# Optimization experiments

Measured on AMD Instinct MI355X. Metric: run time of the kernel, lower is better.

The kernel has to match this reference:

```python
import jax, jax.numpy as jnp
import numpy as np
import math

EMB, QK, V, HEAD = 512, 64, 64, 8
B, S = 8, 2048

def setup_inputs() -> dict:
    key = jax.random.key(0)
    ks = jax.random.split(key, 10)
    sc = 1.0 / math.sqrt(EMB)
    return {
        "x_q": jax.random.normal(ks[0], (B, S, EMB), jnp.float32),
        "x_k_v": jax.random.normal(ks[1], (B, S, EMB), jnp.float32),
        "attn_mask": jax.random.randint(ks[2], (B, S, S), 0, 2, jnp.int32),
        "w_q": jax.random.normal(ks[3], (HEAD * QK, EMB), jnp.float32) * sc,
        "b_q": jax.random.normal(ks[4], (HEAD * QK,), jnp.float32) * sc,
        "w_k": jax.random.normal(ks[5], (HEAD * QK, EMB), jnp.float32) * sc,
        "b_k": jax.random.normal(ks[6], (HEAD * QK,), jnp.float32) * sc,
        "w_v": jax.random.normal(ks[7], (HEAD * V, EMB), jnp.float32) * sc,
        "b_v": jax.random.normal(ks[8], (HEAD * V,), jnp.float32) * sc,
    }

def reference(x_q, x_k_v, attn_mask, w_q, b_q, w_k, b_k, w_v, b_v):
    Bq, Sq, _ = x_q.shape
    Skv = x_k_v.shape[1]
    # linear projections (torch Linear: x @ W.T + b)
    q = (x_q @ w_q.T + b_q).reshape(Bq, Sq, HEAD, QK)     # [B,Sq,H,Dk]
    k = (x_k_v @ w_k.T + b_k).reshape(Bq, Skv, HEAD, QK)  # [B,Skv,H,Dk]
    v = (x_k_v @ w_v.T + b_v).reshape(Bq, Skv, HEAD, V)   # [B,Skv,H,Dv]
    # scores [B,H,Sq,Skv]
    attn = jnp.einsum("bqhd,bkhd->bhqk", q, k) / math.sqrt(QK)
    mask = attn_mask[:, None, :, :].astype(bool)
    attn = jnp.where(mask, jnp.float32(-1e9), attn)
    attn = jax.nn.softmax(attn, axis=-1)
    z = jnp.einsum("bhqk,bkhd->bqhd", attn, v)            # [B,Sq,H,Dv]
    return z.reshape(Bq, Sq, HEAD * V)
```

## Files before the change

### kernel.cpp

```cpp
#include <hip/hip_runtime.h>
#include <hip/hip_bf16.h>
#include <math.h>

typedef float  f32x4  __attribute__((ext_vector_type(4)));
typedef float  f32x16 __attribute__((ext_vector_type(16)));
typedef short  s16x8  __attribute__((ext_vector_type(8)));
typedef __bf16 bf16x8 __attribute__((ext_vector_type(8)));
typedef unsigned int u32;
typedef unsigned int u32x4 __attribute__((ext_vector_type(4)));
typedef unsigned short u16;
typedef unsigned long long u64;

#define DEVI static __device__ __forceinline__

#if defined(__has_builtin) && __has_builtin(__builtin_amdgcn_exp2f)
#define EXP2(x) __builtin_amdgcn_exp2f(x)
#else
#define EXP2(x) exp2f(x)
#endif

DEVI u32 cvtpk(float lo, float hi) {
  u32 r;
  asm("v_cvt_pk_bf16_f32 %0, %1, %2" : "=v"(r) : "v"(lo), "v"(hi));
  return r;
}

DEVI f32x4 mfma_bf16(s16x8 a, s16x8 b, f32x4 c) {
  return __builtin_amdgcn_mfma_f32_16x16x32_bf16(
      __builtin_bit_cast(bf16x8, a), __builtin_bit_cast(bf16x8, b), c, 0, 0, 0);
}

DEVI f32x16 mfma32(s16x8 a, s16x8 b, f32x16 c) {
  return __builtin_amdgcn_mfma_f32_32x32x16_bf16(
      __builtin_bit_cast(bf16x8, a), __builtin_bit_cast(bf16x8, b), c, 0, 0, 0);
}

DEVI void gload_lds16(const void* g, void* l) {
  __builtin_amdgcn_global_load_lds(
      (const __attribute__((address_space(1))) void*)g,
      (__attribute__((address_space(3))) void*)l, 16, 0, 0);
}

__global__ __launch_bounds__(256)
void mask_pack(const int* __restrict__ mask, u64* __restrict__ mp,
               const float* __restrict__ wq, const float* __restrict__ wk,
               const float* __restrict__ wv, u16* __restrict__ Wbf) {
  const int t = threadIdx.x, lane = t & 63;
  if (blockIdx.x >= 8192) {
    const u32 blk = blockIdx.x - 8192;
    const u32 g0 = blk * 4096 + (u32)t * 16;
    const u32 mtx = g0 >> 18;
    const float* src = (mtx == 0) ? wq : (mtx == 1 ? wk : wv);
    const u32 idx = g0 & 262143u;
    #pragma unroll
    for (int i = 0; i < 2; ++i) {
      f32x4 v0 = *(const f32x4*)(src + idx + i * 8);
      f32x4 v1 = *(const f32x4*)(src + idx + i * 8 + 4);
      u32x4 pk;
      pk[0] = cvtpk(v0[0], v0[1]); pk[1] = cvtpk(v0[2], v0[3]);
      pk[2] = cvtpk(v1[0], v1[1]); pk[3] = cvtpk(v1[2], v1[3]);
      *(u32x4*)(Wbf + (size_t)mtx * 262144 + idx + i * 8) = pk;
    }
    return;
  }
  const u32 gw = blockIdx.x * 4 + (t >> 6);
  const u32 W0 = gw * 16;
  #define MSRC(W) ((((size_t)((W) >> 16) * 2048 + ((W) & 2047u)) * 2048) \
                   + (((W) >> 11) & 31u) * 64 + lane)
  int c0 = mask[MSRC(W0)];
  int c1 = mask[MSRC(W0 + 1)];
  #pragma unroll 4
  for (u32 k = 0; k < 16; ++k) {
    u64 bits = __ballot(c0 == 0);
    if (lane == 0) mp[W0 + k] = bits;
    c0 = c1;
    if (k + 2 < 16) c1 = mask[MSRC(W0 + k + 2)];
  }
  #undef MSRC
}

__global__ __launch_bounds__(256, 2)
void qkv_proj(const float* __restrict__ xq, const float* __restrict__ xkv,
              const u16* __restrict__ Wbf,
              const float* __restrict__ bq, const float* __restrict__ bk,
              const float* __restrict__ bv,
              u16* __restrict__ Qo, u16* __restrict__ Ko, u16* __restrict__ VTo)
{
  __shared__ __align__(16) char smem[57344];
  char* a32 = smem;
  char* bbf = smem + 32768;
  char* abf = smem + 49152;

  const int t = threadIdx.x, lane = t & 63, w = t >> 6;
  const int z = blockIdx.z;
  const float* X  = (z == 0) ? xq : xkv;
  const u16*   W  = Wbf + (size_t)z * 262144;
  const float* Bv = (z == 0) ? bq : (z == 1 ? bk : bv);

  const int m0 = blockIdx.x * 128, n0 = blockIdx.y * 128;
  const int wr = w >> 1, wc = w & 1, g = lane >> 4, q15 = lane & 15;
  const int srow = t >> 1, shalf = t & 1;

  f32x4 acc[4][4];
  #pragma unroll
  for (int i = 0; i < 4; ++i)
    #pragma unroll
    for (int j = 0; j < 4; ++j) acc[i][j] = (f32x4){0.f, 0.f, 0.f, 0.f};

  const float* aSrc[4];
  int aDst[4];
  #pragma unroll
  for (int i = 0; i < 4; ++i) {
    int c = w * 256 + i * 64 + lane;
    int r = c >> 3, s = c & 7, j = s ^ (r & 7);
    aSrc[i] = X + (size_t)(m0 + r) * 512 + j * 4;
    aDst[i] = (w * 256 + i * 64) * 16;
  }
  const u16* bSrc[2];
  int bDst[2];
  #pragma unroll
  for (int i = 0; i < 2; ++i) {
    int c = i * 256 + w * 64 + lane;
    int r = c >> 2, s = c & 3, j = s ^ (r & 3);
    bSrc[i] = W + (size_t)(n0 + r) * 512 + j * 8;
    bDst[i] = (i * 256 + w * 64) * 16;
  }

  #pragma unroll
  for (int i = 0; i < 4; ++i) gload_lds16(aSrc[i], a32 + aDst[i]);
  #pragma unroll
  for (int i = 0; i < 2; ++i) gload_lds16(bSrc[i], bbf + bDst[i]);
  asm volatile("" ::: "memory");

  const int wbyte = srow * 64;
  const int sw = (srow & 3) << 4;

  #pragma unroll 1
  for (int kt = 0; kt < 16; ++kt) {
    const int cur = kt & 1;
    if (kt + 1 < 16) {
      #pragma unroll
      for (int i = 0; i < 4; ++i) {
        aSrc[i] += 32;
        gload_lds16(aSrc[i], a32 + (cur ^ 1) * 16384 + aDst[i]);
      }
      #pragma unroll
      for (int i = 0; i < 2; ++i) {
        bSrc[i] += 32;
        gload_lds16(bSrc[i], bbf + (cur ^ 1) * 8192 + bDst[i]);
      }
      asm volatile("" ::: "memory");
      asm volatile("s_waitcnt vmcnt(6)" ::: "memory");
    } else {
      asm volatile("s_waitcnt vmcnt(0)" ::: "memory");
    }
    asm volatile("s_waitcnt lgkmcnt(0)" ::: "memory");
    __builtin_amdgcn_sched_barrier(0);
    asm volatile("s_barrier" ::: "memory");

    {
      const char* base = a32 + cur * 16384 + srow * 128;
      f32x4 av[4];
      #pragma unroll
      for (int jj = 0; jj < 4; ++jj) {
        int slot = (shalf * 4 + jj) ^ (srow & 7);
        av[jj] = *(const f32x4*)(base + slot * 16);
      }
      const float* pf = (const float*)av;
      #pragma unroll
      for (int half = 0; half < 2; ++half) {
        u32x4 wa;
        #pragma unroll
        for (int e2 = 0; e2 < 4; ++e2)
          wa[e2] = cvtpk(pf[half * 8 + 2 * e2], pf[half * 8 + 2 * e2 + 1]);
        *(u32x4*)(abf + wbyte + ((shalf * 32 + half * 16) ^ sw)) = wa;
      }
    }
    asm volatile("s_waitcnt lgkmcnt(0)" ::: "memory");
    __builtin_amdgcn_sched_barrier(0);
    asm volatile("s_barrier" ::: "memory");

    s16x8 afr[4], bfr[4];
    #pragma unroll
    for (int mi = 0; mi < 4; ++mi) {
      int row = wr * 64 + mi * 16 + q15;
      afr[mi] = *(const s16x8*)(abf + row * 64 + ((g * 16) ^ ((row & 3) << 4)));
    }
    #pragma unroll
    for (int ni = 0; ni < 4; ++ni) {
      int row = wc * 64 + ni * 16 + q15;
      bfr[ni] = *(const s16x8*)(bbf + cur * 8192 + row * 64 + ((g * 16) ^ ((row & 3) << 4)));
    }
    #pragma unroll
    for (int mi = 0; mi < 4; ++mi)
      #pragma unroll
      for (int ni = 0; ni < 4; ++ni)
        acc[mi][ni] = mfma_bf16(afr[mi], bfr[ni], acc[mi][ni]);
  }

  float bias[4];
  #pragma unroll
  for (int ni = 0; ni < 4; ++ni) bias[ni] = Bv[n0 + wc * 64 + ni * 16 + q15];

  if (z < 2) {
    u16* Out = z ? Ko : Qo;
    const float scale = z ? 1.0f : 0.18033688011112042f;
    #pragma unroll
    for (int mi = 0; mi < 4; ++mi)
      #pragma unroll
      for (int ni = 0; ni < 4; ++ni)
        #pragma unroll
        for (int r = 0; r < 4; r += 2) {
          int m = m0 + wr * 64 + mi * 16 + g * 4 + r;
          int n = n0 + wc * 64 + ni * 16 + q15;
          u32 pk = cvtpk((acc[mi][ni][r] + bias[ni]) * scale,
                         (acc[mi][ni][r + 1] + bias[ni]) * scale);
          Out[(size_t)m * 512 + n]       = (u16)pk;
          Out[(size_t)(m + 1) * 512 + n] = (u16)(pk >> 16);
        }
  } else {
    __syncthreads();
    #pragma unroll
    for (int mi = 0; mi < 4; ++mi)
      #pragma unroll
      for (int ni = 0; ni < 4; ++ni)
        #pragma unroll
        for (int r = 0; r < 4; r += 2) {
          int ml = wr * 64 + mi * 16 + g * 4 + r;
          int nl = wc * 64 + ni * 16 + q15;
          *(u32*)(smem + nl * 272 + ml * 2) =
              cvtpk(acc[mi][ni][r] + bias[ni], acc[mi][ni][r + 1] + bias[ni]);
        }
    __syncthreads();
    const int b  = m0 >> 11;
    const int s0 = m0 & 2047;
    #pragma unroll
    for (int nn = 0; nn < 2; ++nn) {
      int n  = nn * 64 + (t >> 2);
      int q4 = t & 3;
      u16* dst = VTo + (size_t)(b * 512 + n0 + n) * 2048 + s0 + q4 * 32;
      #pragma unroll
      for (int jj = 0; jj < 4; ++jj)
        *(s16x8*)(dst + jj * 8) = *(const s16x8*)(smem + n * 272 + q4 * 64 + jj * 16);
    }
  }
}

__global__ __launch_bounds__(256, 2)
void attn_fwd(const u16* __restrict__ Q, const u16* __restrict__ K,
              const u16* __restrict__ VT, const u64* __restrict__ MP,
              float* __restrict__ out)
{
  __shared__ __align__(16) char lds_k[2][16384];
  __shared__ __align__(16) char lds_v[2][2][8192];

  const int bid = blockIdx.x;
  const int hh = bid & 7, b = (bid >> 3) & 7, qt = bid >> 6;
  const int t = threadIdx.x, lane = t & 63, w = t >> 6;
  const int l31 = lane & 31, hi = lane >> 5;
  const int qbase = qt * 128 + w * 32;
  const int swz = (l31 & 7) << 4;

  s16x8 qf[4];
  #pragma unroll
  for (int j = 0; j < 4; ++j)
    qf[j] = *(const s16x8*)(Q + (size_t)(b * 2048 + qbase + l31) * 512
                              + hh * 64 + j * 16 + hi * 8);
  asm volatile("" ::: "memory");

  f32x16 o0 = {0.f,0.f,0.f,0.f,0.f,0.f,0.f,0.f,0.f,0.f,0.f,0.f,0.f,0.f,0.f,0.f};
  f32x16 o1 = o0, o2 = o0;
  const f32x16 ZZ = o0;
  const s16x8 onesf = {0x3F80,0x3F80,0x3F80,0x3F80,0x3F80,0x3F80,0x3F80,0x3F80};

  const int srow8 = lane >> 3, slot = lane & 7;

  const u16* kP[4];
  int kD[4];
  #pragma unroll
  for (int i = 0; i < 4; ++i) {
    int rl = w * 32 + i * 8 + srow8;
    kP[i] = K + (size_t)(b * 2048 + rl) * 512 + hh * 64 + (slot ^ (rl & 7)) * 8;
    kD[i] = (w * 32 + i * 8) * 128;
  }
  const u16* vP[2];
  int vD[2];
  #pragma unroll
  for (int i = 0; i < 2; ++i) {
    int d = w * 16 + i * 8 + srow8;
    vP[i] = VT + (size_t)(b * 512 + hh * 64 + d) * 2048 + (slot ^ (d & 7)) * 8;
    vD[i] = (w * 16 + i * 8) * 128;
  }
  const u64* mpP = MP + (size_t)b * 32 * 2048 + qbase + l31;

  #pragma unroll
  for (int i = 0; i < 4; ++i) gload_lds16(kP[i], &lds_k[0][kD[i]]);
  #pragma unroll
  for (int hf = 0; hf < 2; ++hf)
    #pragma unroll
    for (int i = 0; i < 2; ++i)
      gload_lds16(vP[i] + hf * 64, &lds_v[0][hf][vD[i]]);
  asm volatile("" ::: "memory");
  u64 pm0 = mpP[0], pm1 = mpP[2048];

#define HALF(KB, VB, KW) do {                                                  \
    f32x16 p0 = ZZ, p1 = ZZ;                                                   \
    _Pragma("unroll")                                                          \
    for (int j = 0; j < 4; ++j) {                                              \
      s16x8 a0 = *(const s16x8*)((KB) + l31 * 128        + ((j * 32 + hi * 16) ^ swz)); \
      s16x8 a1 = *(const s16x8*)((KB) + (l31 + 32) * 128 + ((j * 32 + hi * 16) ^ swz)); \
      p0 = mfma32(a0, qf[j], p0);                                              \
      p1 = mfma32(a1, qf[j], p1);                                              \
    }                                                                          \
    u64 kws = (KW) >> (hi * 4);                                                \
    u32 mm0 = (u32)kws, mm1 = (u32)(kws >> 32);                                \
    u32 wds[16];                                                               \
    _Pragma("unroll")                                                          \
    for (int t2 = 0; t2 < 2; ++t2) {                                           \
      const u32 mmw = t2 ? mm1 : mm0;                                          \
      _Pragma("unroll")                                                        \
      for (int q2 = 0; q2 < 8; ++q2) {                                         \
        const int bp = 8 * (q2 >> 1) + 2 * (q2 & 1);                           \
        float s0v = t2 ? p1[2 * q2] : p0[2 * q2];                              \
        float s1v = t2 ? p1[2 * q2 + 1] : p0[2 * q2 + 1];                      \
        float e0 = EXP2(s0v), e1 = EXP2(s1v);                                  \
        u32 k0 = (u32)((int)(mmw << (31 - bp)) >> 31);                         \
        u32 k1 = (u32)((int)(mmw << (30 - bp)) >> 31);                         \
        e0 = __builtin_bit_cast(float, __builtin_bit_cast(u32, e0) & k0);      \
        e1 = __builtin_bit_cast(float, __builtin_bit_cast(u32, e1) & k1);      \
        wds[t2 * 8 + q2] = cvtpk(e0, e1);                                      \
      }                                                                        \
    }                                                                          \
    _Pragma("unroll")                                                          \
    for (int j = 0; j < 4; ++j) {                                              \
      const int ia = 2 * j, ib = 2 * j + 1;                                    \
      u32 wa0 = wds[(ia >> 2) * 8 + 2 * (ia & 3)];                             \
      u32 wa1 = wds[(ia >> 2) * 8 + 2 * (ia & 3) + 1];                         \
      u32 wb0 = wds[(ib >> 2) * 8 + 2 * (ib & 3)];                             \
      u32 wb1 = wds[(ib >> 2) * 8 + 2 * (ib & 3) + 1];                         \
      asm("v_permlane32_swap_b32 %0, %1" : "+v"(wa0), "+v"(wb0));              \
      asm("v_permlane32_swap_b32 %0, %1" : "+v"(wa1), "+v"(wb1));              \
      u32x4 aw = {wa0, wa1, wb0, wb1};                                         \
      s16x8 af = __builtin_bit_cast(s16x8, aw);                                \
      s16x8 v0 = *(const s16x8*)((VB) + l31 * 128        + ((j * 32 + hi * 16) ^ swz)); \
      s16x8 v1 = *(const s16x8*)((VB) + (l31 + 32) * 128 + ((j * 32 + hi * 16) ^ swz)); \
      o0 = mfma32(af, v0, o0);                                                 \
      o1 = mfma32(af, v1, o1);                                                 \
      o2 = mfma32(af, onesf, o2);                                              \
    }                                                                          \
  } while (0)

  #pragma unroll 1
  for (int kt = 0; kt < 16; ++kt) {
    const int cur = kt & 1;
    const u64 kwA = pm0, kwB = pm1;
    if (kt + 1 < 16) {
      #pragma unroll
      for (int i = 0; i < 4; ++i) kP[i] += 65536;
      #pragma unroll
      for (int i = 0; i < 2; ++i) vP[i] += 128;
      mpP += 4096;
      #pragma unroll
      for (int i = 0; i < 4; ++i) gload_lds16(kP[i], &lds_k[cur ^ 1][kD[i]]);
      #pragma unroll
      for (int hf = 0; hf < 2; ++hf)
        #pragma unroll
        for (int i = 0; i < 2; ++i)
          gload_lds16(vP[i] + hf * 64, &lds_v[cur ^ 1][hf][vD[i]]);
      asm volatile("" ::: "memory");
      pm0 = mpP[0]; pm1 = mpP[2048];
      asm volatile("s_waitcnt vmcnt(10)" ::: "memory");
    } else {
      asm volatile("s_waitcnt vmcnt(0)" ::: "memory");
    }
    asm volatile("s_barrier" ::: "memory");

    HALF(&lds_k[cur][0],    &lds_v[cur][0][0], kwA);
    HALF(&lds_k[cur][8192], &lds_v[cur][1][0], kwB);

    asm volatile("s_waitcnt lgkmcnt(0)" ::: "memory");
    __builtin_amdgcn_sched_barrier(0);
    asm volatile("s_barrier" ::: "memory");
  }
#undef HALF

  #pragma unroll
  for (int reg = 0; reg < 16; ++reg) {
    const int ql = (reg & 3) + 8 * (reg >> 2) + 4 * hi;
    const float linv = 1.0f / o2[reg];
    float* po = out + (size_t)(b * 2048 + qbase + ql) * 512 + hh * 64 + l31;
    po[0]  = o0[reg] * linv;
    po[32] = o1[reg] * linv;
  }
}

extern "C" void kernel_launch(void* const* d_in, const int* in_sizes, int n_in,
                              void* d_out, int out_size, void* d_ws, size_t ws_size,
                              hipStream_t stream) {
  const float* xq  = (const float*)d_in[0];
  const float* xkv = (const float*)d_in[1];
  const int*   msk = (const int*)d_in[2];
  const float* wq  = (const float*)d_in[3];
  const float* bq  = (const float*)d_in[4];
  const float* wk  = (const float*)d_in[5];
  const float* bk  = (const float*)d_in[6];
  const float* wv  = (const float*)d_in[7];
  const float* bv  = (const float*)d_in[8];

  u16* Qw  = (u16*)d_ws;
  u16* Kw  = Qw + (size_t)16384 * 512;
  u16* VT  = Kw + (size_t)16384 * 512;
  u64* MP  = (u64*)(VT + (size_t)4096 * 2048);
  u16* Wbf = (u16*)(MP + (size_t)8 * 32 * 2048);

  mask_pack<<<dim3(8384), 256, 0, stream>>>(msk, MP, wq, wk, wv, Wbf);
  qkv_proj<<<dim3(128, 4, 3), 256, 0, stream>>>(xq, xkv, Wbf, bq, bk, bv,
                                                Qw, Kw, VT);
  attn_fwd<<<dim3(1024), 256, 0, stream>>>(Qw, Kw, VT, MP, (float*)d_out);
}
```

Baseline: 197.7 us.

## Pre-expand mask bits into per-lane 16-bit AND words for attention

The mask-pack kernel now writes, for each 64-bit ballot, 32 per-lane u32 words that are already expanded into 0xFFFF/0 halves in the lane order the attention kernel uses. The attention kernel then ANDs the packed bf16 exponent pairs directly with these words. This drops the per-element shift/sign-extend mask extraction from the softmax inner loop, and the vmcnt waits are retuned so the mask loads are waited on only just before use. The cost is a mask buffer 32 times larger, read as 128 bytes per lane per K tile, so both kernels move more memory.

```diff
diff --git a/kernel.cpp b/kernel.cpp
--- a/kernel.cpp
+++ b/kernel.cpp
@@ -42,7 +42,7 @@
 }
 
 __global__ __launch_bounds__(256)
-void mask_pack(const int* __restrict__ mask, u64* __restrict__ mp,
+void mask_pack(const int* __restrict__ mask, u32* __restrict__ MX,
                const float* __restrict__ wq, const float* __restrict__ wk,
                const float* __restrict__ wv, u16* __restrict__ Wbf) {
   const int t = threadIdx.x, lane = t & 63;
@@ -65,6 +65,8 @@
   }
   const u32 gw = blockIdx.x * 4 + (t >> 6);
   const u32 W0 = gw * 16;
+  const int hi2 = (lane >> 4) & 1, w16 = lane & 15;
+  const int bp = 32 * (w16 >> 3) + 8 * ((w16 & 7) >> 1) + 2 * (w16 & 1) + 4 * hi2;
   #define MSRC(W) ((((size_t)((W) >> 16) * 2048 + ((W) & 2047u)) * 2048) \
                    + (((W) >> 11) & 31u) * 64 + lane)
   int c0 = mask[MSRC(W0)];
@@ -72,7 +74,12 @@
   #pragma unroll 4
   for (u32 k = 0; k < 16; ++k) {
     u64 bits = __ballot(c0 == 0);
-    if (lane == 0) mp[W0 + k] = bits;
+    if (lane < 32) {
+      u32 m0 = (u32)(bits >> bp) & 1u;
+      u32 m1 = (u32)(bits >> (bp + 1)) & 1u;
+      u32 wd = (m0 ? 0xFFFFu : 0u) | (m1 ? 0xFFFF0000u : 0u);
+      MX[(size_t)(W0 + k) * 32 + lane] = wd;
+    }
     c0 = c1;
     if (k + 2 < 16) c1 = mask[MSRC(W0 + k + 2)];
   }
@@ -248,7 +255,7 @@
 
 __global__ __launch_bounds__(256, 2)
 void attn_fwd(const u16* __restrict__ Q, const u16* __restrict__ K,
-              const u16* __restrict__ VT, const u64* __restrict__ MP,
+              const u16* __restrict__ VT, const u32* __restrict__ MX,
               float* __restrict__ out)
 {
   __shared__ __align__(16) char lds_k[2][16384];
@@ -291,7 +298,7 @@
     vP[i] = VT + (size_t)(b * 512 + hh * 64 + d) * 2048 + (slot ^ (d & 7)) * 8;
     vD[i] = (w * 16 + i * 8) * 128;
   }
-  const u64* mpP = MP + (size_t)b * 32 * 2048 + qbase + l31;
+  const u32* mxP = MX + ((size_t)(b * 32) * 2048 + qbase + l31) * 32 + hi * 16;
 
   #pragma unroll
   for (int i = 0; i < 4; ++i) gload_lds16(kP[i], &lds_k[0][kD[i]]);
@@ -301,9 +308,8 @@
     for (int i = 0; i < 2; ++i)
       gload_lds16(vP[i] + hf * 64, &lds_v[0][hf][vD[i]]);
   asm volatile("" ::: "memory");
-  u64 pm0 = mpP[0], pm1 = mpP[2048];
-
-#define HALF(KB, VB, KW) do {                                                  \
+
+#define HALF(KB, VB, MW, WAITASM) do {                                         \
     f32x16 p0 = ZZ, p1 = ZZ;                                                   \
     _Pragma("unroll")                                                          \
     for (int j = 0; j < 4; ++j) {                                              \
@@ -312,25 +318,19 @@
       p0 = mfma32(a0, qf[j], p0);                                              \
       p1 = mfma32(a1, qf[j], p1);                                              \
     }                                                                          \
-    u64 kws = (KW) >> (hi * 4);                                                \
-    u32 mm0 = (u32)kws, mm1 = (u32)(kws >> 32);                                \
     u32 wds[16];                                                               \
     _Pragma("unroll")                                                          \
     for (int t2 = 0; t2 < 2; ++t2) {                                           \
-      const u32 mmw = t2 ? mm1 : mm0;                                          \
       _Pragma("unroll")                                                        \
       for (int q2 = 0; q2 < 8; ++q2) {                                         \
-        const int bp = 8 * (q2 >> 1) + 2 * (q2 & 1);                           \
         float s0v = t2 ? p1[2 * q2] : p0[2 * q2];                              \
         float s1v = t2 ? p1[2 * q2 + 1] : p0[2 * q2 + 1];                      \
-        float e0 = EXP2(s0v), e1 = EXP2(s1v);                                  \
-        u32 k0 = (u32)((int)(mmw << (31 - bp)) >> 31);                         \
-        u32 k1 = (u32)((int)(mmw << (30 - bp)) >> 31);                         \
-        e0 = __builtin_bit_cast(float, __builtin_bit_cast(u32, e0) & k0);      \
-        e1 = __builtin_bit_cast(float, __builtin_bit_cast(u32, e1) & k1);      \
-        wds[t2 * 8 + q2] = cvtpk(e0, e1);                                      \
+        wds[t2 * 8 + q2] = cvtpk(EXP2(s0v), EXP2(s1v));                        \
       }                                                                        \
     }                                                                          \
+    asm volatile("s_waitcnt " WAITASM ::: "memory");                           \
+    _Pragma("unroll")                                                          \
+    for (int w16 = 0; w16 < 16; ++w16) wds[w16] &= (MW)[w16 >> 2][w16 & 3];    \
     _Pragma("unroll")                                                          \
     for (int j = 0; j < 4; ++j) {                                              \
       const int ia = 2 * j, ib = 2 * j + 1;                                    \
@@ -353,13 +353,18 @@
   #pragma unroll 1
   for (int kt = 0; kt < 16; ++kt) {
     const int cur = kt & 1;
-    const u64 kwA = pm0, kwB = pm1;
+    u32x4 mwA[4], mwB[4];
+    #pragma unroll
+    for (int i = 0; i < 4; ++i) mwA[i] = *(const u32x4*)(mxP + i * 4);
+    #pragma unroll
+    for (int i = 0; i < 4; ++i) mwB[i] = *(const u32x4*)(mxP + 65536 + i * 4);
+    asm volatile("" ::: "memory");
     if (kt + 1 < 16) {
       #pragma unroll
       for (int i = 0; i < 4; ++i) kP[i] += 65536;
       #pragma unroll
       for (int i = 0; i < 2; ++i) vP[i] += 128;
-      mpP += 4096;
+      mxP += 131072;
       #pragma unroll
       for (int i = 0; i < 4; ++i) gload_lds16(kP[i], &lds_k[cur ^ 1][kD[i]]);
       #pragma unroll
@@ -368,15 +373,19 @@
         for (int i = 0; i < 2; ++i)
           gload_lds16(vP[i] + hf * 64, &lds_v[cur ^ 1][hf][vD[i]]);
       asm volatile("" ::: "memory");
-      pm0 = mpP[0]; pm1 = mpP[2048];
-      asm volatile("s_waitcnt vmcnt(10)" ::: "memory");
+      asm volatile("s_waitcnt vmcnt(16)" ::: "memory");
     } else {
-      asm volatile("s_waitcnt vmcnt(0)" ::: "memory");
+      asm volatile("s_waitcnt vmcnt(8)" ::: "memory");
     }
     asm volatile("s_barrier" ::: "memory");
 
-    HALF(&lds_k[cur][0],    &lds_v[cur][0][0], kwA);
-    HALF(&lds_k[cur][8192], &lds_v[cur][1][0], kwB);
+    if (kt + 1 < 16) {
+      HALF(&lds_k[cur][0],    &lds_v[cur][0][0], mwA, "vmcnt(12)");
+      HALF(&lds_k[cur][8192], &lds_v[cur][1][0], mwB, "vmcnt(8)");
+    } else {
+      HALF(&lds_k[cur][0],    &lds_v[cur][0][0], mwA, "vmcnt(4)");
+      HALF(&lds_k[cur][8192], &lds_v[cur][1][0], mwB, "vmcnt(0)");
+    }
 
     asm volatile("s_waitcnt lgkmcnt(0)" ::: "memory");
     __builtin_amdgcn_sched_barrier(0);
@@ -410,11 +419,11 @@
   u16* Qw  = (u16*)d_ws;
   u16* Kw  = Qw + (size_t)16384 * 512;
   u16* VT  = Kw + (size_t)16384 * 512;
-  u64* MP  = (u64*)(VT + (size_t)4096 * 2048);
-  u16* Wbf = (u16*)(MP + (size_t)8 * 32 * 2048);
-
-  mask_pack<<<dim3(8384), 256, 0, stream>>>(msk, MP, wq, wk, wv, Wbf);
+  u32* MX  = (u32*)(VT + (size_t)4096 * 2048);
+  u16* Wbf = (u16*)(MX + (size_t)8 * 32 * 2048 * 32);
+
+  mask_pack<<<dim3(8384), 256, 0, stream>>>(msk, MX, wq, wk, wv, Wbf);
   qkv_proj<<<dim3(128, 4, 3), 256, 0, stream>>>(xq, xkv, Wbf, bq, bk, bv,
                                                 Qw, Kw, VT);
-  attn_fwd<<<dim3(1024), 256, 0, stream>>>(Qw, Kw, VT, MP, (float*)d_out);
-}
+  attn_fwd<<<dim3(1024), 256, 0, stream>>>(Qw, Kw, VT, MX, (float*)d_out);
+}
```

After: 224.6 us. +13.6%, slower.
